# Kernel tuning notes

Hardware: AMD Instinct MI355X
Metric: run time of the kernel (lower is better)

Reference implementation:

```python
import jax, jax.numpy as jnp
import numpy as np

B, T, D, K = 8, 1024, 256, 100
G, V = 2, 320
TEMP = 0.1
DIV_W = 0.1
L2_W = 10.0
DIV_EPS = 1e-7
COS_EPS = 1e-8


def setup_inputs() -> dict:
    key = jax.random.key(0)
    k1, k2, k3, k4, k5 = jax.random.split(key, 5)
    return {
        "quantized_features": jax.random.normal(k1, (B, T, D), jnp.float32),
        "context_features": jax.random.normal(k2, (B, T, D), jnp.float32),
        "codebook_logits": jax.random.normal(k3, (B, T, G, V), jnp.float32),
        "neg_idx": jax.random.randint(k4, (B, T, K), 0, T, jnp.int32),
        "mask": jax.random.bernoulli(k5, 0.5, (B, T)),
    }


def _losses(quantized_features, context_features, codebook_logits, neg_idx, mask):
    Bq, Tq, Dq = quantized_features.shape
    # --- contrastive loss ---
    # gather negatives: [B, T, K, D]
    negatives = quantized_features[jnp.arange(Bq)[:, None, None], neg_idx]
    # targets = [positive, negatives]: [B, T, K+1, D]
    targets = jnp.concatenate([quantized_features[:, :, None, :], negatives], axis=2)
    pred = context_features[:, :, None, :]  # [B, T, 1, D]
    dot = jnp.sum(pred * targets, axis=-1)  # [B, T, K+1]
    pn = jnp.sqrt(jnp.sum(pred * pred, axis=-1))      # [B, T, 1]
    tn = jnp.sqrt(jnp.sum(targets * targets, axis=-1))  # [B, T, K+1]
    cos = dot / jnp.maximum(pn * tn, COS_EPS)
    # kill positive-as-negative collisions (column 0 is the true positive)
    pos_is_neg = neg_idx == jnp.arange(Tq)[None, :, None]  # [B, T, K]
    collision = jnp.concatenate(
        [jnp.zeros((Bq, Tq, 1), dtype=bool), pos_is_neg], axis=2)
    logits = jnp.where(collision, -jnp.inf, cos) / TEMP
    # cross-entropy with target class 0, reduction='sum', over masked positions only
    logp0 = jax.nn.log_softmax(logits, axis=-1)[..., 0]  # [B, T]
    loss_c = -jnp.sum(jnp.where(mask, logp0, 0.0))

    # --- diversity loss ---
    probs = jax.nn.softmax(codebook_logits.astype(jnp.float32), axis=-1)  # [B,T,G,V]
    avg = probs.reshape(Bq * Tq, G, V).mean(axis=0)  # [G, V]
    entropy = -jnp.sum(avg * jnp.log(avg + DIV_EPS), axis=-1)  # [G]
    perplexity = jnp.exp(entropy)
    loss_d = jnp.sum(V - perplexity)

    # --- l2 norm loss ---
    loss_l2 = jnp.mean(quantized_features.astype(jnp.float32) ** 2)

    loss = loss_c + DIV_W * loss_d + L2_W * loss_l2
    return loss


def reference(quantized_features, context_features, codebook_logits, neg_idx, mask):
    return _losses(quantized_features, context_features, codebook_logits, neg_idx, mask)
```

## Files before the change

kernel.cpp:

```cpp
#include <hip/hip_runtime.h>
#include <hip/hip_bf16.h>
#include <math.h>

#define B_ 8
#define T_ 1024
#define D_ 256
#define K_ 100
#define G_ 2
#define V_ 320
#define NT_ 101
#define TEMP_ 0.1f
#define DIV_W_ 0.1f
#define L2_W_ 10.0f
#define DIV_EPS_ 1e-7f
#define COS_EPS_ 1e-8f

#define WS_AVG   2
#define WS_FLAG  643
#define WS_SSQ   644
#define WS_ZERO_TOP WS_SSQ
#define WS_LOSSP 17408
#define WS_QBF16 25600
#define WS_BF16_BYTES ((size_t)(WS_QBF16 + (size_t)B_ * T_ * D_ / 2) * 4)

#define NORM_BLOCKS 512
#define CB_BLOCKS   256

__device__ inline unsigned short f2bf_rne(float f) {
    unsigned int u = __float_as_uint(f);
    u += 0x7FFFu + ((u >> 16) & 1u);
    return (unsigned short)(u >> 16);
}

template <bool PACK_BF16>
__global__ __launch_bounds__(256) void prep_kernel(
    const float* __restrict__ q, const float* __restrict__ cb,
    const unsigned int* __restrict__ maskw, float* __restrict__ ws)
{
    __shared__ float sh[G_ * V_];
    __shared__ int sA, sB;
    const int tid = threadIdx.x;
    const int lane = tid & 63;
    const int wavein = tid >> 6;
    const int blk = blockIdx.x;

    if (blk < NORM_BLOCKS) {
        const int b = blk & 7;
        const int seg = blk >> 3;
        float ssq = 0.0f;
#pragma unroll
        for (int i = 0; i < 4; i++) {
            const int r = b * T_ + seg * 16 + wavein * 4 + i;
            const float4 v = ((const float4*)(q + (size_t)r * D_))[lane];
            ssq += v.x * v.x + v.y * v.y + v.z * v.z + v.w * v.w;
            if (PACK_BF16) {
                ushort4 pk;
                pk.x = f2bf_rne(v.x); pk.y = f2bf_rne(v.y);
                pk.z = f2bf_rne(v.z); pk.w = f2bf_rne(v.w);
                ((ushort4*)((char*)ws + (size_t)WS_QBF16 * 4 +
                            (size_t)r * 512))[lane] = pk;
            }
        }
#pragma unroll
        for (int sft = 32; sft >= 1; sft >>= 1) ssq += __shfl_xor(ssq, sft);
        if (lane == 0) sh[wavein] = ssq;
        __syncthreads();
        if (tid == 0)
            ws[WS_SSQ + blk] = sh[0] + sh[1] + sh[2] + sh[3];

        if (blk == 0) {
            if (tid == 0) { sA = 0; sB = 0; }
            __syncthreads();
            int a = 0, bb = 0;
            for (int i = tid; i < (B_ * T_) / 4; i += 256) {
                const unsigned int w = maskw[i];
                a  |= (w > 1u) ? 1 : 0;
                bb |= (w != 0u && w != 0x3F800000u) ? 1 : 0;
            }
            if (a)  atomicOr(&sA, 1);
            if (bb) atomicOr(&sB, 1);
            __syncthreads();
            if (tid == 0)
                ((int*)ws)[WS_FLAG] = (!sA) ? 0 : ((!sB) ? 1 : 2);
        }
    } else {
        for (int i = tid; i < G_ * V_; i += 256) sh[i] = 0.0f;
        __syncthreads();
        const int cblk = blk - NORM_BLOCKS;
        const int base = cblk * 4 + wavein;
        float r0[5] = {0, 0, 0, 0, 0};
        float r1[5] = {0, 0, 0, 0, 0};
        const bool odd = (base & 1);
#pragma unroll 1
        for (int i = 0; i < 16; i++) {
            const int r = base + 1024 * i;
            const float* row = cb + (size_t)r * V_;
            float v[5];
#pragma unroll
            for (int j = 0; j < 5; j++)
                v[j] = __builtin_nontemporal_load(&row[lane + 64 * j]);
            float mx = fmaxf(fmaxf(fmaxf(v[0], v[1]), fmaxf(v[2], v[3])), v[4]);
#pragma unroll
            for (int s = 32; s >= 1; s >>= 1) mx = fmaxf(mx, __shfl_xor(mx, s));
            float e[5], sum = 0.0f;
#pragma unroll
            for (int j = 0; j < 5; j++) { e[j] = __expf(v[j] - mx); sum += e[j]; }
#pragma unroll
            for (int s = 32; s >= 1; s >>= 1) sum += __shfl_xor(sum, s);
            const float is = 1.0f / sum;
            if (odd) {
#pragma unroll
                for (int j = 0; j < 5; j++) r1[j] += e[j] * is;
            } else {
#pragma unroll
                for (int j = 0; j < 5; j++) r0[j] += e[j] * is;
            }
        }
#pragma unroll
        for (int j = 0; j < 5; j++) {
            atomicAdd(&sh[0 * V_ + lane + 64 * j], r0[j]);
            atomicAdd(&sh[1 * V_ + lane + 64 * j], r1[j]);
        }
        __syncthreads();
        for (int i = tid; i < G_ * V_; i += 256)
            atomicAdd(&ws[WS_AVG + i], sh[i]);
    }
}

template <bool USE_BF16>
__global__ __launch_bounds__(256) void contrastive_kernel(
    const float* __restrict__ quant,
    const float* __restrict__ ctx,
    const int* __restrict__ negidx,
    const void* __restrict__ maskp,
    float* __restrict__ ws)
{
    const int cblk = blockIdx.x;
    const int b = cblk & 7;
    const int t = cblk >> 3;
    const int bt = b * T_ + t;

    const int tid = threadIdx.x;
    const int flag = ((const int*)ws)[WS_FLAG];
    bool m;
    if (flag == 2)      m = ((const unsigned char*)maskp)[bt] != 0;
    else if (flag == 1) m = ((const float*)maskp)[bt] != 0.0f;
    else                m = ((const int*)maskp)[bt] != 0;
    if (!m) {
        if (tid == 0) ws[WS_LOSSP + cblk] = 0.0f;
        return;
    }

    __shared__ float s_pred[D_];
    __shared__ float s_pn;
    __shared__ int   s_idx[NT_ + 3];
    __shared__ float s_logit[NT_ + 3];

    if (tid < 64) {
        const float4 v = ((const float4*)(ctx + (size_t)bt * D_))[tid];
        ((float4*)s_pred)[tid] = v;
        float s = v.x * v.x + v.y * v.y + v.z * v.z + v.w * v.w;
#pragma unroll
        for (int sh = 32; sh >= 1; sh >>= 1) s += __shfl_xor(s, sh);
        if (tid == 0) s_pn = sqrtf(s);
    } else if (tid < 64 + K_) {
        s_idx[tid - 63] =
            __builtin_nontemporal_load(&negidx[(size_t)bt * K_ + (tid - 64)]);
    } else if (tid == 64 + K_) {
        s_idx[0] = t;
    }
    __syncthreads();

    const float pn = s_pn;
    const int g = tid >> 2;
    const int p = tid & 3;

#pragma unroll
    for (int pass = 0; pass < 2; ++pass) {
        const int k = g + 64 * pass;
        if (k < NT_) {
            const int idx = s_idx[k];
            float dot = 0.0f, tn2 = 0.0f;
            if (USE_BF16) {
                const uint4* row = (const uint4*)((const char*)ws +
                    (size_t)WS_QBF16 * 4 + (size_t)(b * T_ + idx) * 512);
                uint4 u[8];
#pragma unroll
                for (int i = 0; i < 8; ++i) u[i] = row[i * 4 + p];
#pragma unroll
                for (int i = 0; i < 8; ++i) {
                    const int J0 = (p + 4 * i) * 4;
                    const unsigned int w0 = u[i].x, w1 = u[i].y,
                                       w2 = u[i].z, w3 = u[i].w;
                    const float2 q0 = ((const float2*)s_pred)[J0 + 0];
                    const float2 q1 = ((const float2*)s_pred)[J0 + 1];
                    const float2 q2 = ((const float2*)s_pred)[J0 + 2];
                    const float2 q3 = ((const float2*)s_pred)[J0 + 3];
                    const float a0 = __uint_as_float(w0 << 16);
                    const float a1 = __uint_as_float(w0 & 0xFFFF0000u);
                    const float a2 = __uint_as_float(w1 << 16);
                    const float a3 = __uint_as_float(w1 & 0xFFFF0000u);
                    const float a4 = __uint_as_float(w2 << 16);
                    const float a5 = __uint_as_float(w2 & 0xFFFF0000u);
                    const float a6 = __uint_as_float(w3 << 16);
                    const float a7 = __uint_as_float(w3 & 0xFFFF0000u);
                    dot += a0 * q0.x + a1 * q0.y + a2 * q1.x + a3 * q1.y
                         + a4 * q2.x + a5 * q2.y + a6 * q3.x + a7 * q3.y;
                    tn2 += a0 * a0 + a1 * a1 + a2 * a2 + a3 * a3
                         + a4 * a4 + a5 * a5 + a6 * a6 + a7 * a7;
                }
            } else {
                const float4* row = (const float4*)(quant +
                    ((size_t)b * T_ + idx) * D_);
                float4 r[16];
#pragma unroll
                for (int i = 0; i < 16; ++i) r[i] = row[i * 4 + p];
#pragma unroll
                for (int i = 0; i < 16; ++i) {
                    const float4 q = ((const float4*)s_pred)[i * 4 + p];
                    dot += r[i].x * q.x + r[i].y * q.y
                         + r[i].z * q.z + r[i].w * q.w;
                    tn2 += r[i].x * r[i].x + r[i].y * r[i].y
                         + r[i].z * r[i].z + r[i].w * r[i].w;
                }
            }
            dot += __shfl_xor(dot, 1);
            dot += __shfl_xor(dot, 2);
            tn2 += __shfl_xor(tn2, 1);
            tn2 += __shfl_xor(tn2, 2);
            if (p == 0) {
                s_logit[k] = (k > 0 && idx == t) ? -1e30f
                    : (dot / fmaxf(pn * sqrtf(tn2), COS_EPS_)) * (1.0f / TEMP_);
            }
        }
    }
    __syncthreads();

    if (tid < 64) {
        const float l0 = s_logit[tid];
        const float l1 = (tid + 64 < NT_) ? s_logit[tid + 64] : -1e30f;
        float mx = fmaxf(l0, l1);
#pragma unroll
        for (int s = 32; s >= 1; s >>= 1) mx = fmaxf(mx, __shfl_xor(mx, s));
        float sum = __expf(l0 - mx) + __expf(l1 - mx);
#pragma unroll
        for (int s = 32; s >= 1; s >>= 1) sum += __shfl_xor(sum, s);
        if (tid == 0) {
            const float logp0 = s_logit[0] - (mx + __logf(sum));
            ws[WS_LOSSP + cblk] = -logp0;
        }
    }
}

__global__ __launch_bounds__(256) void finalize_kernel(
    const float* __restrict__ ws, float* __restrict__ out)
{
    __shared__ float sred[4];
    const int tid = threadIdx.x;
    const int lane = tid & 63;
    const int wavein = tid >> 6;

    float lc = 0.0f;
    for (int i = tid; i < B_ * T_; i += 256) lc += ws[WS_LOSSP + i];
#pragma unroll
    for (int s = 32; s >= 1; s >>= 1) lc += __shfl_xor(lc, s);
    if (lane == 0) sred[wavein] = lc;
    __syncthreads();

    if (tid < 64) {
        float ss = 0.0f;
#pragma unroll
        for (int i = 0; i < 8; i++) ss += ws[WS_SSQ + lane + 64 * i];
        const float* avg = ws + WS_AVG;
        float e0 = 0.0f, e1 = 0.0f;
        const float inv = 1.0f / (float)(B_ * T_);
#pragma unroll
        for (int i = 0; i < 5; i++) {
            const float a0 = avg[0 * V_ + lane + 64 * i] * inv;
            const float a1 = avg[1 * V_ + lane + 64 * i] * inv;
            e0 -= a0 * __logf(a0 + DIV_EPS_);
            e1 -= a1 * __logf(a1 + DIV_EPS_);
        }
#pragma unroll
        for (int s = 32; s >= 1; s >>= 1) {
            ss += __shfl_xor(ss, s);
            e0 += __shfl_xor(e0, s);
            e1 += __shfl_xor(e1, s);
        }
        if (tid == 0) {
            const float loss_c = sred[0] + sred[1] + sred[2] + sred[3];
            const float loss_d = ((float)V_ - __expf(e0)) + ((float)V_ - __expf(e1));
            const float loss_l2 = ss / (float)(B_ * T_ * D_);
            out[0] = loss_c + DIV_W_ * loss_d + L2_W_ * loss_l2;
        }
    }
}

extern "C" void kernel_launch(void* const* d_in, const int* in_sizes, int n_in,
                              void* d_out, int out_size, void* d_ws, size_t ws_size,
                              hipStream_t stream) {
    const float* quant = (const float*)d_in[0];
    const float* ctx   = (const float*)d_in[1];
    const float* cb    = (const float*)d_in[2];
    const int*   nidx  = (const int*)d_in[3];
    const void*  mask  = d_in[4];
    float* ws  = (float*)d_ws;
    float* out = (float*)d_out;

    const bool bf16 = (ws_size >= WS_BF16_BYTES);

    hipMemsetAsync(d_ws, 0, (WS_ZERO_TOP) * sizeof(float), stream);

    if (bf16) {
        prep_kernel<true><<<NORM_BLOCKS + CB_BLOCKS, 256, 0, stream>>>(
            quant, cb, (const unsigned int*)mask, ws);
        contrastive_kernel<true><<<B_ * T_, 256, 0, stream>>>(
            quant, ctx, nidx, mask, ws);
    } else {
        prep_kernel<false><<<NORM_BLOCKS + CB_BLOCKS, 256, 0, stream>>>(
            quant, cb, (const unsigned int*)mask, ws);
        contrastive_kernel<false><<<B_ * T_, 256, 0, stream>>>(
            quant, ctx, nidx, mask, ws);
    }
    finalize_kernel<<<1, 256, 0, stream>>>(ws, out);
}
```

Before: 136.5 us.

## Move codebook softmax into contrastive launch and drop workspace memset

The codebook-softmax diversity blocks move out of the prep kernel and become the first blocks of the contrastive kernel. The prep kernel now only does the bf16 pack and the squared-norm sums, so it gets shorter and the softmax work overlaps with the contrastive blocks. In the large-workspace path each codebook block writes its own partial histogram, which the finalize kernel reduces. This removes the global atomics and the memset launch, at the cost of finalize reading 256×640 partials serially. The negative-index load also drops its nontemporal hint.

```diff
diff --git a/kernel.cpp b/kernel.cpp
--- a/kernel.cpp
+++ b/kernel.cpp
@@ -15,15 +15,14 @@
 #define DIV_EPS_ 1e-7f
 #define COS_EPS_ 1e-8f
 
-#define WS_AVG   2
-#define WS_FLAG  643
-#define WS_SSQ   644
-#define WS_ZERO_TOP WS_SSQ
-#define WS_LOSSP 17408
-#define WS_QBF16 25600
-#define WS_BF16_BYTES ((size_t)(WS_QBF16 + (size_t)B_ * T_ * D_ / 2) * 4)
-
-#define NORM_BLOCKS 512
+#define WS_FLAG  0
+#define WS_SSQ   64
+#define WS_LOSSP 1024
+#define WS_CBP   9216
+#define WS_QBF16 173056
+#define WS_BIG_BYTES ((size_t)(WS_QBF16 + (size_t)B_ * T_ * D_ / 2) * 4)
+
+#define PACK_BLOCKS 512
 #define CB_BLOCKS   256
 
 __device__ inline unsigned short f2bf_rne(float f) {
@@ -32,62 +31,76 @@
     return (unsigned short)(u >> 16);
 }
 
-template <bool PACK_BF16>
+template <bool PACK>
 __global__ __launch_bounds__(256) void prep_kernel(
-    const float* __restrict__ q, const float* __restrict__ cb,
-    const unsigned int* __restrict__ maskw, float* __restrict__ ws)
+    const float* __restrict__ q, const unsigned int* __restrict__ maskw,
+    float* __restrict__ ws)
 {
-    __shared__ float sh[G_ * V_];
+    __shared__ float sh[4];
     __shared__ int sA, sB;
     const int tid = threadIdx.x;
     const int lane = tid & 63;
     const int wavein = tid >> 6;
     const int blk = blockIdx.x;
-
-    if (blk < NORM_BLOCKS) {
-        const int b = blk & 7;
-        const int seg = blk >> 3;
-        float ssq = 0.0f;
-#pragma unroll
-        for (int i = 0; i < 4; i++) {
-            const int r = b * T_ + seg * 16 + wavein * 4 + i;
-            const float4 v = ((const float4*)(q + (size_t)r * D_))[lane];
-            ssq += v.x * v.x + v.y * v.y + v.z * v.z + v.w * v.w;
-            if (PACK_BF16) {
-                ushort4 pk;
-                pk.x = f2bf_rne(v.x); pk.y = f2bf_rne(v.y);
-                pk.z = f2bf_rne(v.z); pk.w = f2bf_rne(v.w);
-                ((ushort4*)((char*)ws + (size_t)WS_QBF16 * 4 +
-                            (size_t)r * 512))[lane] = pk;
-            }
-        }
-#pragma unroll
-        for (int sft = 32; sft >= 1; sft >>= 1) ssq += __shfl_xor(ssq, sft);
-        if (lane == 0) sh[wavein] = ssq;
+    const int b = blk & 7;
+    const int seg = blk >> 3;
+
+    float ssq = 0.0f;
+#pragma unroll
+    for (int i = 0; i < 4; i++) {
+        const int r = b * T_ + seg * 16 + wavein * 4 + i;
+        const float4 v = ((const float4*)(q + (size_t)r * D_))[lane];
+        ssq += v.x * v.x + v.y * v.y + v.z * v.z + v.w * v.w;
+        if (PACK) {
+            ushort4 pk;
+            pk.x = f2bf_rne(v.x); pk.y = f2bf_rne(v.y);
+            pk.z = f2bf_rne(v.z); pk.w = f2bf_rne(v.w);
+            ((ushort4*)((char*)ws + (size_t)WS_QBF16 * 4 +
+                        (size_t)r * 512))[lane] = pk;
+        }
+    }
+#pragma unroll
+    for (int sft = 32; sft >= 1; sft >>= 1) ssq += __shfl_xor(ssq, sft);
+    if (lane == 0) sh[wavein] = ssq;
+    __syncthreads();
+    if (tid == 0)
+        ws[WS_SSQ + blk] = sh[0] + sh[1] + sh[2] + sh[3];
+
+    if (blk == 0) {
+        if (tid == 0) { sA = 0; sB = 0; }
+        __syncthreads();
+        int a = 0, bb = 0;
+        for (int i = tid; i < (B_ * T_) / 4; i += 256) {
+            const unsigned int w = maskw[i];
+            a  |= (w > 1u) ? 1 : 0;
+            bb |= (w != 0u && w != 0x3F800000u) ? 1 : 0;
+        }
+        if (a)  atomicOr(&sA, 1);
+        if (bb) atomicOr(&sB, 1);
         __syncthreads();
         if (tid == 0)
-            ws[WS_SSQ + blk] = sh[0] + sh[1] + sh[2] + sh[3];
-
-        if (blk == 0) {
-            if (tid == 0) { sA = 0; sB = 0; }
-            __syncthreads();
-            int a = 0, bb = 0;
-            for (int i = tid; i < (B_ * T_) / 4; i += 256) {
-                const unsigned int w = maskw[i];
-                a  |= (w > 1u) ? 1 : 0;
-                bb |= (w != 0u && w != 0x3F800000u) ? 1 : 0;
-            }
-            if (a)  atomicOr(&sA, 1);
-            if (bb) atomicOr(&sB, 1);
-            __syncthreads();
-            if (tid == 0)
-                ((int*)ws)[WS_FLAG] = (!sA) ? 0 : ((!sB) ? 1 : 2);
-        }
-    } else {
+            ((int*)ws)[WS_FLAG] = (!sA) ? 0 : ((!sB) ? 1 : 2);
+    }
+}
+
+template <bool BIG>
+__global__ __launch_bounds__(256) void main_kernel(
+    const float* __restrict__ quant,
+    const float* __restrict__ ctx,
+    const float* __restrict__ cb,
+    const int* __restrict__ negidx,
+    const void* __restrict__ maskp,
+    float* __restrict__ ws)
+{
+    const int tid = threadIdx.x;
+    const int lane = tid & 63;
+    const int wavein = tid >> 6;
+
+    if (blockIdx.x < CB_BLOCKS) {
+        __shared__ float sh[G_ * V_];
         for (int i = tid; i < G_ * V_; i += 256) sh[i] = 0.0f;
         __syncthreads();
-        const int cblk = blk - NORM_BLOCKS;
-        const int base = cblk * 4 + wavein;
+        const int base = blockIdx.x * 4 + wavein;
         float r0[5] = {0, 0, 0, 0, 0};
         float r1[5] = {0, 0, 0, 0, 0};
         const bool odd = (base & 1);
@@ -122,25 +135,21 @@
             atomicAdd(&sh[1 * V_ + lane + 64 * j], r1[j]);
         }
         __syncthreads();
-        for (int i = tid; i < G_ * V_; i += 256)
-            atomicAdd(&ws[WS_AVG + i], sh[i]);
-    }
-}
-
-template <bool USE_BF16>
-__global__ __launch_bounds__(256) void contrastive_kernel(
-    const float* __restrict__ quant,
-    const float* __restrict__ ctx,
-    const int* __restrict__ negidx,
-    const void* __restrict__ maskp,
-    float* __restrict__ ws)
-{
-    const int cblk = blockIdx.x;
+        if (BIG) {
+            float* rec = ws + WS_CBP + (size_t)blockIdx.x * (G_ * V_);
+            for (int i = tid; i < G_ * V_; i += 256) rec[i] = sh[i];
+        } else {
+            for (int i = tid; i < G_ * V_; i += 256)
+                atomicAdd(&ws[WS_CBP + i], sh[i]);
+        }
+        return;
+    }
+
+    const int cblk = blockIdx.x - CB_BLOCKS;
     const int b = cblk & 7;
     const int t = cblk >> 3;
     const int bt = b * T_ + t;
 
-    const int tid = threadIdx.x;
     const int flag = ((const int*)ws)[WS_FLAG];
     bool m;
     if (flag == 2)      m = ((const unsigned char*)maskp)[bt] != 0;
@@ -164,8 +173,7 @@
         for (int sh = 32; sh >= 1; sh >>= 1) s += __shfl_xor(s, sh);
         if (tid == 0) s_pn = sqrtf(s);
     } else if (tid < 64 + K_) {
-        s_idx[tid - 63] =
-            __builtin_nontemporal_load(&negidx[(size_t)bt * K_ + (tid - 64)]);
+        s_idx[tid - 63] = negidx[(size_t)bt * K_ + (tid - 64)];
     } else if (tid == 64 + K_) {
         s_idx[0] = t;
     }
@@ -181,7 +189,7 @@
         if (k < NT_) {
             const int idx = s_idx[k];
             float dot = 0.0f, tn2 = 0.0f;
-            if (USE_BF16) {
+            if (BIG) {
                 const uint4* row = (const uint4*)((const char*)ws +
                     (size_t)WS_QBF16 * 4 + (size_t)(b * T_ + idx) * 512);
                 uint4 u[8];
@@ -252,45 +260,55 @@
     }
 }
 
+template <int NREC>
 __global__ __launch_bounds__(256) void finalize_kernel(
     const float* __restrict__ ws, float* __restrict__ out)
 {
-    __shared__ float sred[4];
+    __shared__ float s_avg[G_ * V_];
+    __shared__ float sl[4], sq[4];
     const int tid = threadIdx.x;
     const int lane = tid & 63;
     const int wavein = tid >> 6;
 
+    for (int pos = tid; pos < G_ * V_; pos += 256) {
+        float a = 0.0f;
+#pragma unroll 4
+        for (int r = 0; r < NREC; ++r)
+            a += ws[WS_CBP + (size_t)r * (G_ * V_) + pos];
+        s_avg[pos] = a;
+    }
     float lc = 0.0f;
     for (int i = tid; i < B_ * T_; i += 256) lc += ws[WS_LOSSP + i];
-#pragma unroll
-    for (int s = 32; s >= 1; s >>= 1) lc += __shfl_xor(lc, s);
-    if (lane == 0) sred[wavein] = lc;
+    float ss = 0.0f;
+    for (int i = tid; i < PACK_BLOCKS; i += 256) ss += ws[WS_SSQ + i];
+#pragma unroll
+    for (int s = 32; s >= 1; s >>= 1) {
+        lc += __shfl_xor(lc, s);
+        ss += __shfl_xor(ss, s);
+    }
+    if (lane == 0) { sl[wavein] = lc; sq[wavein] = ss; }
     __syncthreads();
 
     if (tid < 64) {
-        float ss = 0.0f;
-#pragma unroll
-        for (int i = 0; i < 8; i++) ss += ws[WS_SSQ + lane + 64 * i];
-        const float* avg = ws + WS_AVG;
         float e0 = 0.0f, e1 = 0.0f;
         const float inv = 1.0f / (float)(B_ * T_);
 #pragma unroll
         for (int i = 0; i < 5; i++) {
-            const float a0 = avg[0 * V_ + lane + 64 * i] * inv;
-            const float a1 = avg[1 * V_ + lane + 64 * i] * inv;
+            const float a0 = s_avg[0 * V_ + lane + 64 * i] * inv;
+            const float a1 = s_avg[1 * V_ + lane + 64 * i] * inv;
             e0 -= a0 * __logf(a0 + DIV_EPS_);
             e1 -= a1 * __logf(a1 + DIV_EPS_);
         }
 #pragma unroll
         for (int s = 32; s >= 1; s >>= 1) {
-            ss += __shfl_xor(ss, s);
             e0 += __shfl_xor(e0, s);
             e1 += __shfl_xor(e1, s);
         }
         if (tid == 0) {
-            const float loss_c = sred[0] + sred[1] + sred[2] + sred[3];
+            const float loss_c = sl[0] + sl[1] + sl[2] + sl[3];
+            const float ssqt   = sq[0] + sq[1] + sq[2] + sq[3];
             const float loss_d = ((float)V_ - __expf(e0)) + ((float)V_ - __expf(e1));
-            const float loss_l2 = ss / (float)(B_ * T_ * D_);
+            const float loss_l2 = ssqt / (float)(B_ * T_ * D_);
             out[0] = loss_c + DIV_W_ * loss_d + L2_W_ * loss_l2;
         }
     }
@@ -307,20 +325,20 @@
     float* ws  = (float*)d_ws;
     float* out = (float*)d_out;
 
-    const bool bf16 = (ws_size >= WS_BF16_BYTES);
-
-    hipMemsetAsync(d_ws, 0, (WS_ZERO_TOP) * sizeof(float), stream);
-
-    if (bf16) {
-        prep_kernel<true><<<NORM_BLOCKS + CB_BLOCKS, 256, 0, stream>>>(
-            quant, cb, (const unsigned int*)mask, ws);
-        contrastive_kernel<true><<<B_ * T_, 256, 0, stream>>>(
-            quant, ctx, nidx, mask, ws);
+    const bool big = (ws_size >= WS_BIG_BYTES);
+
+    if (big) {
+        prep_kernel<true><<<PACK_BLOCKS, 256, 0, stream>>>(
+            quant, (const unsigned int*)mask, ws);
+        main_kernel<true><<<CB_BLOCKS + B_ * T_, 256, 0, stream>>>(
+            quant, ctx, cb, nidx, mask, ws);
+        finalize_kernel<CB_BLOCKS><<<1, 256, 0, stream>>>(ws, out);
     } else {
-        prep_kernel<false><<<NORM_BLOCKS + CB_BLOCKS, 256, 0, stream>>>(
-            quant, cb, (const unsigned int*)mask, ws);
-        contrastive_kernel<false><<<B_ * T_, 256, 0, stream>>>(
-            quant, ctx, nidx, mask, ws);
-    }
-    finalize_kernel<<<1, 256, 0, stream>>>(ws, out);
-}
+        hipMemsetAsync(ws + WS_CBP, 0, G_ * V_ * sizeof(float), stream);
+        prep_kernel<false><<<PACK_BLOCKS, 256, 0, stream>>>(
+            quant, (const unsigned int*)mask, ws);
+        main_kernel<false><<<CB_BLOCKS + B_ * T_, 256, 0, stream>>>(
+            quant, ctx, cb, nidx, mask, ws);
+        finalize_kernel<1><<<1, 256, 0, stream>>>(ws, out);
+    }
+}
```

New measurement: 183.2 us. 1.34x slower.
